# Performance work log

Measured on AMD Instinct MI355X. Metric: run time of the kernel, lower is better.

Reference implementation:

```python
import jax, jax.numpy as jnp
import numpy as np

B, N, H, E = 8, 2048, 4, 64  # batch, nodes, heads, embedding_dim (= GAT out_channels)
NEG_SLOPE = 0.2


def setup_inputs() -> dict:
    key = jax.random.key(0)
    ks = jax.random.split(key, 12)
    state = jax.random.normal(ks[0], (B, N), dtype=jnp.float32)
    strucEmb = jax.random.normal(ks[1], (N, E), dtype=jnp.float32) * 0.1
    # adjacency mask: True where NO edge (masked_fill -inf). Keep self-loops so every row has an edge.
    no_edge = jax.random.uniform(ks[2], (N, N)) > 0.02
    adj_mask = no_edge.at[jnp.arange(N), jnp.arange(N)].set(False)
    g = lambda k, shp: jax.random.normal(k, shp, dtype=jnp.float32) * np.float32(np.sqrt(2.0 / sum(shp[-2:])))
    W_gat = g(ks[3], (1, H * E))          # torch Linear(1, H*E, bias=False) weight.T laid out as (in,out)
    att = g(ks[4], (H, 2 * E, 1))         # GAT additive attention params
    Ws = g(ks[5], (E, E))                 # weight_struc (out,in)
    Wst = g(ks[6], (E, E))                # weight_state (out,in)
    lin1_w = g(ks[7], (E, E)); lin1_b = jnp.zeros((E,), jnp.float32)
    lin2_w = g(ks[8], (E, E)); lin2_b = jnp.zeros((E,), jnp.float32)
    lin3_w = g(ks[9], (1, 2 * E)); lin3_b = jnp.zeros((1,), jnp.float32)
    return dict(state=state, strucEmb=strucEmb, adj_mask=adj_mask, W_gat=W_gat, att=att,
                Ws=Ws, Wst=Wst, lin1_w=lin1_w, lin1_b=lin1_b, lin2_w=lin2_w, lin2_b=lin2_b,
                lin3_w=lin3_w, lin3_b=lin3_b)


def reference(state, strucEmb, adj_mask, W_gat, att, Ws, Wst,
              lin1_w, lin1_b, lin2_w, lin2_b, lin3_w, lin3_b):
    # --- Custom_GATConv_v2 ---
    # reshaped_state: [B,N,1]; Wh = state @ W -> [B,N,H*E] -> [B,H,N,E]
    Wh = (state[..., None] @ W_gat).reshape(B, N, H, E).transpose(0, 2, 1, 3)
    a_src = att[:, :E, 0]   # [H,E]
    a_tgt = att[:, E:, 0]   # [H,E]
    src = jnp.einsum('bhne,he->bhn', Wh, a_src)
    tgt = jnp.einsum('bhne,he->bhn', Wh, a_tgt)
    e = src[:, :, :, None] + tgt[:, :, None, :]          # [B,H,N,N]
    e = jnp.where(e > 0, e, NEG_SLOPE * e)               # LeakyReLU
    e = jnp.where(adj_mask[None, None], -jnp.inf, e)     # mask non-edges
    attn = jax.nn.softmax(e, axis=-1)
    x = jnp.einsum('bhij,bhje->bhie', attn, Wh).mean(axis=1)  # [B,N,E]

    # --- DeepQNet head (is_for_learn=True branch) ---
    x = jax.nn.relu(strucEmb @ Ws.T + x @ Wst.T)         # [B,N,E]
    state_emb = x.sum(axis=1)                            # [B,E]
    beta_state = state_emb @ lin1_w.T + lin1_b           # [B,E]
    beta_action = x @ lin2_w.T + lin2_b                  # [B,N,E]
    expand_state = jnp.broadcast_to(beta_state[:, None, :], (B, N, E))
    out = jax.nn.relu(jnp.concatenate([expand_state, beta_action], axis=2))  # [B,N,2E]
    return out @ lin3_w.T + lin3_b                       # [B,N,1]
```

## Files before the change

kernel.cpp:

```cpp
#include <hip/hip_runtime.h>

#define BB 8
#define NN 2048
#define HH 4
#define EE 64
#define MAXJ 128
#define NEG 0.2f
#define NCHUNK 32

static constexpr int OFF_CSRC  = 0;
static constexpr int OFF_CTGT  = 4;
static constexpr int OFF_WGWST = 8;
static constexpr int OFF_S     = 264;
static constexpr int OFF_SWS   = 288;
static constexpr int OFF_SATT  = OFF_SWS + NN * EE;
static constexpr int OFF_PART  = OFF_SATT + NN * 32;

__global__ __launch_bounds__(256) void k_sws(const float* __restrict__ strucEmb,
                                             const float* __restrict__ Ws,
                                             const float* __restrict__ W_gat,
                                             const float* __restrict__ att,
                                             const float* __restrict__ Wst,
                                             float* __restrict__ ws) {
    __shared__ float s_wsT[EE * 65];
    __shared__ float s_emb[16 * EE];
    const int t = threadIdx.x;
    const int w = t >> 6, lane = t & 63;
    const int i0 = blockIdx.x * 16;
    for (int k = t; k < EE * EE; k += 256)
        s_wsT[(k & 63) * 65 + (k >> 6)] = Ws[k];
    for (int k = t; k < 16 * EE; k += 256)
        s_emb[k] = strucEmb[(size_t)i0 * EE + k];
    __syncthreads();
    for (int q = 0; q < 4; ++q) {
        int r = w * 4 + q;
        float v = s_emb[r * EE + lane];
        float acc = 0.f;
        for (int e = 0; e < EE; ++e)
            acc += __shfl(v, e) * s_wsT[e * 65 + lane];
        ws[OFF_SWS + (size_t)(i0 + r) * EE + lane] = acc;
    }
    if (blockIdx.x == 0) {
        int h = t >> 6, f = t & 63;
        float acc = 0.f;
        for (int e = 0; e < EE; ++e) acc += W_gat[h * EE + e] * Wst[f * EE + e];
        ws[OFF_WGWST + t] = acc;
        if (t < 2 * HH) {
            int hh = t & 3;
            const float* wgx = W_gat + hh * EE;
            const float* av  = att + hh * 2 * EE + (t >= HH ? EE : 0);
            float a2 = 0.f;
            for (int e = 0; e < EE; ++e) a2 += wgx[e] * av[e];
            if (t < HH) ws[OFF_CSRC + hh] = a2; else ws[OFF_CTGT + hh] = a2;
        }
    }
}

__global__ __launch_bounds__(256) void k_fsatt(const int* __restrict__ adj,
                                               const float* __restrict__ state,
                                               float* __restrict__ ws) {
    __shared__ int   s_jq[4][MAXJ];
    __shared__ int   s_c[4];
    __shared__ int   s_jl[MAXJ];
    __shared__ int   s_cnt;
    __shared__ float s_y[BB * MAXJ];
    const int i = blockIdx.x;
    const int t = threadIdx.x;
    const int w = t >> 6, lane = t & 63;

    {
        const int4* a4 = (const int4*)(adj + (size_t)i * NN) + w * 128;
        int base = 0;
        const unsigned long long below = (1ull << lane) - 1ull;
        for (int q = 0; q < 2; ++q) {
            int4 v = a4[q * 64 + lane];
            int j0 = w * 512 + (q * 64 + lane) * 4;
            int eb = (v.x == 0 ? 1 : 0) | (v.y == 0 ? 2 : 0) |
                     (v.z == 0 ? 4 : 0) | (v.w == 0 ? 8 : 0);
            unsigned long long b0 = __ballot(eb & 1), b1 = __ballot(eb & 2);
            unsigned long long b2 = __ballot(eb & 4), b3 = __ballot(eb & 8);
            int pos = base + __popcll(b0 & below) + __popcll(b1 & below)
                           + __popcll(b2 & below) + __popcll(b3 & below);
            if (eb & 1) { if (pos < MAXJ) s_jq[w][pos] = j0 + 0; ++pos; }
            if (eb & 2) { if (pos < MAXJ) s_jq[w][pos] = j0 + 1; ++pos; }
            if (eb & 4) { if (pos < MAXJ) s_jq[w][pos] = j0 + 2; ++pos; }
            if (eb & 8) { if (pos < MAXJ) s_jq[w][pos] = j0 + 3; ++pos; }
            base += __popcll(b0) + __popcll(b1) + __popcll(b2) + __popcll(b3);
        }
        if (lane == 0) s_c[w] = base > MAXJ ? MAXJ : base;
    }
    __syncthreads();
    {
        int start = 0;
        for (int q = 0; q < w; ++q) start += s_c[q];
        int cw = s_c[w];
        for (int k = lane; k < cw; k += 64) {
            int p = start + k;
            if (p < MAXJ) s_jl[p] = s_jq[w][k];
        }
        if (t == 0) {
            int tot = s_c[0] + s_c[1] + s_c[2] + s_c[3];
            s_cnt = tot > MAXJ ? MAXJ : tot;
        }
    }
    __syncthreads();
    const int cnt = s_cnt;

    for (int x = t; x < BB * MAXJ; x += 256) {
        int k = x & (MAXJ - 1);
        if (k < cnt) s_y[x] = state[(x >> 7) * NN + s_jl[k]];
    }
    __syncthreads();

    int g = t >> 3, k0 = t & 7, b = g >> 2, h = g & 3;
    const float* yb = s_y + b * MAXJ;
    float ct = ws[OFF_CTGT + h];
    float si = state[b * NN + i] * ws[OFF_CSRC + h];
    float mmax = -1e30f;
    for (int k = k0; k < cnt; k += 8) {
        float e = si + ct * yb[k]; e = e > 0.f ? e : NEG * e;
        mmax = fmaxf(mmax, e);
    }
    for (int o = 4; o; o >>= 1) mmax = fmaxf(mmax, __shfl_xor(mmax, o, 8));
    float den = 0.f, num = 0.f;
    for (int k = k0; k < cnt; k += 8) {
        float y = yb[k];
        float e = si + ct * y; e = e > 0.f ? e : NEG * e;
        float p = expf(e - mmax);
        den += p; num += p * y;
    }
    for (int o = 4; o; o >>= 1) { den += __shfl_xor(den, o, 8); num += __shfl_xor(num, o, 8); }
    if (k0 == 0) ws[OFF_SATT + i * 32 + g] = num / den;
}

__global__ void k_se(float* __restrict__ ws) {
    int b = blockIdx.x & 7, chunk = blockIdx.x >> 3;
    int t = threadIdx.x;
    int f = t & 63, sl = t >> 6;
    float wgw[HH];
    for (int h = 0; h < HH; ++h) wgw[h] = 0.25f * ws[OFF_WGWST + h * EE + f];
    float acc = 0.f;
    int i0 = chunk * (NN / NCHUNK);
    for (int i = i0 + sl; i < i0 + NN / NCHUNK; i += 4) {
        float v = ws[OFF_SWS + i * EE + f];
        for (int h = 0; h < HH; ++h)
            v += ws[OFF_SATT + i * 32 + b * 4 + h] * wgw[h];
        acc += fmaxf(v, 0.f);
    }
    __shared__ float red[256];
    red[t] = acc;
    __syncthreads();
    if (t < EE)
        ws[OFF_PART + (size_t)blockIdx.x * EE + t] =
            red[t] + red[t + 64] + red[t + 128] + red[t + 192];
}

__global__ void k_S(const float* __restrict__ lin1_w, const float* __restrict__ lin1_b,
                    const float* __restrict__ lin3_w, const float* __restrict__ lin3_b,
                    float* __restrict__ ws) {
    int b = blockIdx.x;
    int t = threadIdx.x;
    __shared__ float s_l1T[EE * 65];
    __shared__ float s_se[EE];
    for (int it = 0; it < EE; ++it)
        s_l1T[t * 65 + it] = lin1_w[it * EE + t];
    float se = 0.f;
    for (int c = 0; c < NCHUNK; ++c)
        se += ws[OFF_PART + (size_t)(c * BB + b) * EE + t];
    s_se[t] = se;
    __syncthreads();
    float bs = lin1_b[t];
    for (int f2 = 0; f2 < EE; ++f2) bs += s_se[f2] * s_l1T[f2 * 65 + t];
    float r = fmaxf(bs, 0.f) * lin3_w[t];
    for (int o = 32; o; o >>= 1) r += __shfl_xor(r, o);
    if (t == 0) ws[OFF_S + b] = r + lin3_b[0];
}

__global__ __launch_bounds__(256) void k_out3(const float* __restrict__ lin2_w,
                                              const float* __restrict__ lin2_b,
                                              const float* __restrict__ lin3_w,
                                              const float* __restrict__ ws,
                                              float* __restrict__ out) {
    __shared__ float s_l2T[EE * 65];
    __shared__ float s_wgw[HH * EE];
    __shared__ float s_S[BB];
    __shared__ float s_l2b[EE], s_l3[EE];
    const int t = threadIdx.x;
    const int w = t >> 6, lane = t & 63;
    for (int k = t; k < EE * EE; k += 256) {
        int fp = k >> 6, f = k & 63;
        s_l2T[f * 65 + fp] = lin2_w[k];
    }
    s_wgw[t] = 0.25f * ws[OFF_WGWST + t];
    if (t < BB) s_S[t] = ws[OFF_S + t];
    if (t < EE) { s_l2b[t] = lin2_b[t]; s_l3[t] = lin3_w[EE + t]; }
    __syncthreads();

    float lr[EE];
    #pragma unroll
    for (int f = 0; f < EE; ++f) lr[f] = s_l2T[f * 65 + lane];

    const int i = blockIdx.x * 4 + w;
    float xsws = ws[OFF_SWS + (size_t)i * EE + lane];
    float sa = (lane < 32) ? ws[OFF_SATT + i * 32 + lane] : 0.f;
    for (int b = 0; b < BB; ++b) {
        float xv = xsws;
        for (int h = 0; h < HH; ++h)
            xv += __shfl(sa, b * 4 + h) * s_wgw[h * EE + lane];
        xv = fmaxf(xv, 0.f);
        float acc = s_l2b[lane];
        #pragma unroll
        for (int f = 0; f < EE; ++f) acc += __shfl(xv, f) * lr[f];
        float r = fmaxf(acc, 0.f) * s_l3[lane];
        for (int o = 32; o; o >>= 1) r += __shfl_xor(r, o);
        if (lane == 0) out[(size_t)b * NN + i] = s_S[b] + r;
    }
}

extern "C" void kernel_launch(void* const* d_in, const int* in_sizes, int n_in,
                              void* d_out, int out_size, void* d_ws, size_t ws_size,
                              hipStream_t stream) {
    const float* state    = (const float*)d_in[0];
    const float* strucEmb = (const float*)d_in[1];
    const int*   adj      = (const int*)d_in[2];
    const float* W_gat    = (const float*)d_in[3];
    const float* att      = (const float*)d_in[4];
    const float* Ws       = (const float*)d_in[5];
    const float* Wst      = (const float*)d_in[6];
    const float* lin1_w   = (const float*)d_in[7];
    const float* lin1_b   = (const float*)d_in[8];
    const float* lin2_w   = (const float*)d_in[9];
    const float* lin2_b   = (const float*)d_in[10];
    const float* lin3_w   = (const float*)d_in[11];
    const float* lin3_b   = (const float*)d_in[12];
    float* ws = (float*)d_ws;
    float* out = (float*)d_out;

    k_sws  <<<dim3(NN / 16),     dim3(256), 0, stream>>>(strucEmb, Ws, W_gat, att, Wst, ws);
    k_fsatt<<<dim3(NN),          dim3(256), 0, stream>>>(adj, state, ws);
    k_se   <<<dim3(NCHUNK * BB), dim3(256), 0, stream>>>(ws);
    k_S    <<<dim3(BB),          dim3(64),  0, stream>>>(lin1_w, lin1_b, lin3_w, lin3_b, ws);
    k_out3 <<<dim3(NN / 4),      dim3(256), 0, stream>>>(lin2_w, lin2_b, lin3_w, ws, out);
}
```

Measured before the change: 48.14 us.

## Merge front kernels and fold lin1 state head into output kernel

Fuses the strucEmb@Ws kernel and the sparse attention kernel into one launch by assigning extra blocks to the projection work. Each attention block now computes the per-head src/tgt coefficients itself, so it no longer reads them from workspace. The tiny lin1 state-head kernel is removed, and every output block redundantly sums the chunk partials and computes the per-batch scalar. This cuts two kernel launches and their inter-kernel gaps, at the cost of redundant lin1 work and larger shared memory use in each of the 512 output blocks.

Measured after the change: 46.01 us. -4.4%, faster.

```diff
diff --git a/kernel.cpp b/kernel.cpp
--- a/kernel.cpp
+++ b/kernel.cpp
@@ -7,67 +7,67 @@
 #define MAXJ 128
 #define NEG 0.2f
 #define NCHUNK 32
-
-static constexpr int OFF_CSRC  = 0;
-static constexpr int OFF_CTGT  = 4;
+#define NSWSB 128
+
 static constexpr int OFF_WGWST = 8;
-static constexpr int OFF_S     = 264;
 static constexpr int OFF_SWS   = 288;
 static constexpr int OFF_SATT  = OFF_SWS + NN * EE;
 static constexpr int OFF_PART  = OFF_SATT + NN * 32;
 
-__global__ __launch_bounds__(256) void k_sws(const float* __restrict__ strucEmb,
-                                             const float* __restrict__ Ws,
-                                             const float* __restrict__ W_gat,
-                                             const float* __restrict__ att,
-                                             const float* __restrict__ Wst,
-                                             float* __restrict__ ws) {
-    __shared__ float s_wsT[EE * 65];
-    __shared__ float s_emb[16 * EE];
+__global__ __launch_bounds__(256) void k_front(const int* __restrict__ adj,
+                                               const float* __restrict__ state,
+                                               const float* __restrict__ strucEmb,
+                                               const float* __restrict__ Ws,
+                                               const float* __restrict__ W_gat,
+                                               const float* __restrict__ att,
+                                               const float* __restrict__ Wst,
+                                               float* __restrict__ ws) {
+    __shared__ float s_u[EE * 65 + 16 * EE];
+    __shared__ float s_cs[HH], s_ct[HH];
+    __shared__ int   s_c[4];
+    __shared__ int   s_cnt;
     const int t = threadIdx.x;
     const int w = t >> 6, lane = t & 63;
-    const int i0 = blockIdx.x * 16;
-    for (int k = t; k < EE * EE; k += 256)
-        s_wsT[(k & 63) * 65 + (k >> 6)] = Ws[k];
-    for (int k = t; k < 16 * EE; k += 256)
-        s_emb[k] = strucEmb[(size_t)i0 * EE + k];
-    __syncthreads();
-    for (int q = 0; q < 4; ++q) {
-        int r = w * 4 + q;
-        float v = s_emb[r * EE + lane];
-        float acc = 0.f;
-        for (int e = 0; e < EE; ++e)
-            acc += __shfl(v, e) * s_wsT[e * 65 + lane];
-        ws[OFF_SWS + (size_t)(i0 + r) * EE + lane] = acc;
-    }
-    if (blockIdx.x == 0) {
-        int h = t >> 6, f = t & 63;
-        float acc = 0.f;
-        for (int e = 0; e < EE; ++e) acc += W_gat[h * EE + e] * Wst[f * EE + e];
-        ws[OFF_WGWST + t] = acc;
-        if (t < 2 * HH) {
-            int hh = t & 3;
-            const float* wgx = W_gat + hh * EE;
-            const float* av  = att + hh * 2 * EE + (t >= HH ? EE : 0);
-            float a2 = 0.f;
-            for (int e = 0; e < EE; ++e) a2 += wgx[e] * av[e];
-            if (t < HH) ws[OFF_CSRC + hh] = a2; else ws[OFF_CTGT + hh] = a2;
-        }
-    }
-}
-
-__global__ __launch_bounds__(256) void k_fsatt(const int* __restrict__ adj,
-                                               const float* __restrict__ state,
-                                               float* __restrict__ ws) {
-    __shared__ int   s_jq[4][MAXJ];
-    __shared__ int   s_c[4];
-    __shared__ int   s_jl[MAXJ];
-    __shared__ int   s_cnt;
-    __shared__ float s_y[BB * MAXJ];
+
+    if (blockIdx.x >= NN) {
+        float* s_wsT = s_u;
+        float* s_emb = s_u + EE * 65;
+        const int i0 = (blockIdx.x - NN) * 16;
+        for (int k = t; k < EE * EE; k += 256)
+            s_wsT[(k & 63) * 65 + (k >> 6)] = Ws[k];
+        for (int k = t; k < 16 * EE; k += 256)
+            s_emb[k] = strucEmb[(size_t)i0 * EE + k];
+        __syncthreads();
+        for (int q = 0; q < 4; ++q) {
+            int r = w * 4 + q;
+            float v = s_emb[r * EE + lane];
+            float acc = 0.f;
+            for (int e = 0; e < EE; ++e)
+                acc += __shfl(v, e) * s_wsT[e * 65 + lane];
+            ws[OFF_SWS + (size_t)(i0 + r) * EE + lane] = acc;
+        }
+        if (blockIdx.x == NN) {
+            int h = t >> 6, f = t & 63;
+            float acc = 0.f;
+            for (int e = 0; e < EE; ++e) acc += W_gat[h * EE + e] * Wst[f * EE + e];
+            ws[OFF_WGWST + t] = acc;
+        }
+        return;
+    }
+
+    int*   jq = (int*)s_u;
+    int*   jl = (int*)s_u + 4 * MAXJ;
+    float* yy = s_u + 5 * MAXJ;
     const int i = blockIdx.x;
-    const int t = threadIdx.x;
-    const int w = t >> 6, lane = t & 63;
-
+
+    if (t < 2 * HH) {
+        int h = t & 3;
+        const float* wgx = W_gat + h * EE;
+        const float* av  = att + h * 2 * EE + (t >= HH ? EE : 0);
+        float a2 = 0.f;
+        for (int e = 0; e < EE; ++e) a2 += wgx[e] * av[e];
+        if (t < HH) s_cs[h] = a2; else s_ct[h] = a2;
+    }
     {
         const int4* a4 = (const int4*)(adj + (size_t)i * NN) + w * 128;
         int base = 0;
@@ -81,10 +81,10 @@
             unsigned long long b2 = __ballot(eb & 4), b3 = __ballot(eb & 8);
             int pos = base + __popcll(b0 & below) + __popcll(b1 & below)
                            + __popcll(b2 & below) + __popcll(b3 & below);
-            if (eb & 1) { if (pos < MAXJ) s_jq[w][pos] = j0 + 0; ++pos; }
-            if (eb & 2) { if (pos < MAXJ) s_jq[w][pos] = j0 + 1; ++pos; }
-            if (eb & 4) { if (pos < MAXJ) s_jq[w][pos] = j0 + 2; ++pos; }
-            if (eb & 8) { if (pos < MAXJ) s_jq[w][pos] = j0 + 3; ++pos; }
+            if (eb & 1) { if (pos < MAXJ) jq[w * MAXJ + pos] = j0 + 0; ++pos; }
+            if (eb & 2) { if (pos < MAXJ) jq[w * MAXJ + pos] = j0 + 1; ++pos; }
+            if (eb & 4) { if (pos < MAXJ) jq[w * MAXJ + pos] = j0 + 2; ++pos; }
+            if (eb & 8) { if (pos < MAXJ) jq[w * MAXJ + pos] = j0 + 3; ++pos; }
             base += __popcll(b0) + __popcll(b1) + __popcll(b2) + __popcll(b3);
         }
         if (lane == 0) s_c[w] = base > MAXJ ? MAXJ : base;
@@ -96,7 +96,7 @@
         int cw = s_c[w];
         for (int k = lane; k < cw; k += 64) {
             int p = start + k;
-            if (p < MAXJ) s_jl[p] = s_jq[w][k];
+            if (p < MAXJ) jl[p] = jq[w * MAXJ + k];
         }
         if (t == 0) {
             int tot = s_c[0] + s_c[1] + s_c[2] + s_c[3];
@@ -108,14 +108,14 @@
 
     for (int x = t; x < BB * MAXJ; x += 256) {
         int k = x & (MAXJ - 1);
-        if (k < cnt) s_y[x] = state[(x >> 7) * NN + s_jl[k]];
+        if (k < cnt) yy[x] = state[(x >> 7) * NN + jl[k]];
     }
     __syncthreads();
 
     int g = t >> 3, k0 = t & 7, b = g >> 2, h = g & 3;
-    const float* yb = s_y + b * MAXJ;
-    float ct = ws[OFF_CTGT + h];
-    float si = state[b * NN + i] * ws[OFF_CSRC + h];
+    const float* yb = yy + b * MAXJ;
+    float ct = s_ct[h];
+    float si = state[b * NN + i] * s_cs[h];
     float mmax = -1e30f;
     for (int k = k0; k < cnt; k += 8) {
         float e = si + ct * yb[k]; e = e > 0.f ? e : NEG * e;
@@ -155,45 +155,45 @@
             red[t] + red[t + 64] + red[t + 128] + red[t + 192];
 }
 
-__global__ void k_S(const float* __restrict__ lin1_w, const float* __restrict__ lin1_b,
-                    const float* __restrict__ lin3_w, const float* __restrict__ lin3_b,
-                    float* __restrict__ ws) {
-    int b = blockIdx.x;
-    int t = threadIdx.x;
-    __shared__ float s_l1T[EE * 65];
-    __shared__ float s_se[EE];
-    for (int it = 0; it < EE; ++it)
-        s_l1T[t * 65 + it] = lin1_w[it * EE + t];
-    float se = 0.f;
-    for (int c = 0; c < NCHUNK; ++c)
-        se += ws[OFF_PART + (size_t)(c * BB + b) * EE + t];
-    s_se[t] = se;
-    __syncthreads();
-    float bs = lin1_b[t];
-    for (int f2 = 0; f2 < EE; ++f2) bs += s_se[f2] * s_l1T[f2 * 65 + t];
-    float r = fmaxf(bs, 0.f) * lin3_w[t];
-    for (int o = 32; o; o >>= 1) r += __shfl_xor(r, o);
-    if (t == 0) ws[OFF_S + b] = r + lin3_b[0];
-}
-
-__global__ __launch_bounds__(256) void k_out3(const float* __restrict__ lin2_w,
+__global__ __launch_bounds__(256) void k_outS(const float* __restrict__ lin1_w,
+                                              const float* __restrict__ lin1_b,
+                                              const float* __restrict__ lin2_w,
                                               const float* __restrict__ lin2_b,
                                               const float* __restrict__ lin3_w,
+                                              const float* __restrict__ lin3_b,
                                               const float* __restrict__ ws,
                                               float* __restrict__ out) {
+    __shared__ float s_l1T[EE * 65];
     __shared__ float s_l2T[EE * 65];
     __shared__ float s_wgw[HH * EE];
+    __shared__ float s_se[BB * EE];
     __shared__ float s_S[BB];
     __shared__ float s_l2b[EE], s_l3[EE];
     const int t = threadIdx.x;
     const int w = t >> 6, lane = t & 63;
     for (int k = t; k < EE * EE; k += 256) {
-        int fp = k >> 6, f = k & 63;
-        s_l2T[f * 65 + fp] = lin2_w[k];
+        int o = k >> 6, f2 = k & 63;
+        s_l1T[f2 * 65 + o] = lin1_w[k];
+        s_l2T[f2 * 65 + o] = lin2_w[k];
     }
     s_wgw[t] = 0.25f * ws[OFF_WGWST + t];
-    if (t < BB) s_S[t] = ws[OFF_S + t];
     if (t < EE) { s_l2b[t] = lin2_b[t]; s_l3[t] = lin3_w[EE + t]; }
+    for (int p = 0; p < 2; ++p) {
+        int idx = p * 256 + t, b = idx >> 6, f = idx & 63;
+        float se = 0.f;
+        for (int c = 0; c < NCHUNK; ++c)
+            se += ws[OFF_PART + (size_t)(c * BB + b) * EE + f];
+        s_se[idx] = se;
+    }
+    __syncthreads();
+    for (int p = 0; p < 2; ++p) {
+        int b = p * 4 + w;
+        float bs = lin1_b[lane];
+        for (int f2 = 0; f2 < EE; ++f2) bs += s_se[b * EE + f2] * s_l1T[f2 * 65 + lane];
+        float r = fmaxf(bs, 0.f) * lin3_w[lane];
+        for (int o = 32; o; o >>= 1) r += __shfl_xor(r, o);
+        if (lane == 0) s_S[b] = r + lin3_b[0];
+    }
     __syncthreads();
 
     float lr[EE];
@@ -236,9 +236,9 @@
     float* ws = (float*)d_ws;
     float* out = (float*)d_out;
 
-    k_sws  <<<dim3(NN / 16),     dim3(256), 0, stream>>>(strucEmb, Ws, W_gat, att, Wst, ws);
-    k_fsatt<<<dim3(NN),          dim3(256), 0, stream>>>(adj, state, ws);
+    k_front<<<dim3(NN + NSWSB), dim3(256), 0, stream>>>(adj, state, strucEmb, Ws,
+                                                        W_gat, att, Wst, ws);
     k_se   <<<dim3(NCHUNK * BB), dim3(256), 0, stream>>>(ws);
-    k_S    <<<dim3(BB),          dim3(64),  0, stream>>>(lin1_w, lin1_b, lin3_w, lin3_b, ws);
-    k_out3 <<<dim3(NN / 4),      dim3(256), 0, stream>>>(lin2_w, lin2_b, lin3_w, ws, out);
-}
+    k_outS <<<dim3(NN / 4),      dim3(256), 0, stream>>>(lin1_w, lin1_b, lin2_w,
+                                                         lin2_b, lin3_w, lin3_b, ws, out);
+}
```
